# Optimization experiments

Hardware: AMD Instinct MI355X
Metric: run time of the kernel (lower is better)

Reference implementation:

```python
import jax, jax.numpy as jnp
import numpy as np

HIDDEN = 256
N_PROT = 12288
N_MOL = 6144
N_BATCH = 32


def setup_inputs() -> dict:
    key = jax.random.key(0)
    ks = jax.random.split(key, 10)
    s = 1.0 / np.sqrt(HIDDEN)  # torch Linear default init scale
    inp = {
        "prot_embed": jax.random.normal(ks[0], (N_PROT, HIDDEN), jnp.float32),
        "mol_embed": jax.random.normal(ks[1], (N_MOL, HIDDEN), jnp.float32),
        "prot_batch": jnp.sort(jax.random.randint(ks[2], (N_PROT,), 0, N_BATCH)),
        "mol_batch": jnp.sort(jax.random.randint(ks[3], (N_MOL,), 0, N_BATCH)),
        "Wq": jax.random.uniform(ks[4], (HIDDEN, HIDDEN), jnp.float32, -s, s),
        "bq": jax.random.uniform(ks[5], (HIDDEN,), jnp.float32, -s, s),
        "Wk": jax.random.uniform(ks[6], (HIDDEN, HIDDEN), jnp.float32, -s, s),
        "bk": jax.random.uniform(ks[7], (HIDDEN,), jnp.float32, -s, s),
        "Wv": jax.random.uniform(ks[8], (HIDDEN, HIDDEN), jnp.float32, -s, s),
        "bv": jax.random.uniform(ks[9], (HIDDEN,), jnp.float32, -s, s),
    }
    return inp


def reference(prot_embed, mol_embed, prot_batch, mol_batch, Wq, bq, Wk, bk, Wv, bv):
    # Linear projections (torch nn.Linear: x @ W.T + b)
    Q = prot_embed @ Wq.T + bq            # [N, H]
    K = mol_embed @ Wk.T + bk             # [M, H]
    V = mol_embed @ Wv.T + bv             # [M, H]

    scale = 1.0 / jnp.sqrt(jnp.asarray(Q.shape[-1], Q.dtype))
    scores = (Q @ K.T) * scale            # [N, M]

    # block mask: same-batch pairs only
    mask = prot_batch[:, None] == mol_batch[None, :]   # [N, M] bool
    neg_inf = jnp.asarray(-jnp.inf, scores.dtype)
    scores = jnp.where(mask, scores, neg_inf)

    # stable masked softmax; rows with no valid key -> all zeros
    # (matches torch softmax(-inf row) -> nan -> nan_to_num(0.0))
    row_any = mask.any(axis=-1, keepdims=True)
    mx = jnp.max(scores, axis=-1, keepdims=True)
    mx = jnp.where(row_any, mx, 0.0)
    e = jnp.exp(scores - mx)              # exp(-inf)=0 on masked entries
    denom = jnp.sum(e, axis=-1, keepdims=True)
    attn = e / jnp.where(row_any, denom, 1.0)  # [N, M]

    out = attn @ V                        # [N, H]
    return out, attn
```

## Files before the change

### kernel.cpp

```cpp
#include <hip/hip_runtime.h>

#define NPROT 12288
#define NMOL  6144
#define HID   256
#define NB    32

#define PROT_O 0
#define MOL_O  3145728
#define WQ_O   4718592
#define WK_O   4784128
#define WV_O   4849664
#define BQ_O   4915200
#define BK_O   4915456
#define BV_O   4915712
#define Q_O    4915968
#define K_O    8061696
#define VT_O   9634560
#define END_O  11207424

#define FROWS_BLK 49152

typedef __attribute__((ext_vector_type(4))) float f32x4;
typedef __attribute__((ext_vector_type(8))) short bf16x8;
typedef unsigned short u16;
typedef unsigned int   u32;

__device__ __forceinline__ float b2f(u16 u){
  union { u32 i; float f; } v; v.i = ((u32)u) << 16; return v.f;
}
__device__ __forceinline__ u16 f2b(float f){
  union { float fl; u32 i; } v; v.fl = f;
  u32 i = v.i;
  return (u16)((i + 0x7FFFu + ((i >> 16) & 1u)) >> 16);
}

__device__ __forceinline__ void fill_rows8(float* attnf, int fid){
  float* dst = attnf + (size_t)fid * FROWS_BLK + threadIdx.x * 4;
  f32x4 z = {0.f, 0.f, 0.f, 0.f};
  #pragma unroll 4
  for (int i = 0; i < 48; i++)
    __builtin_nontemporal_store(z, (f32x4*)(dst + i * 1024));
}

__global__ __launch_bounds__(256) void convert_kernel(
    const float* __restrict__ prot, const float* __restrict__ mol,
    const float* __restrict__ Wq, const float* __restrict__ Wk,
    const float* __restrict__ Wv, const float* __restrict__ bq,
    const float* __restrict__ bk, const float* __restrict__ bv,
    const int* __restrict__ pb, const int* __restrict__ mb,
    int* __restrict__ rg, u16* __restrict__ cvt, float* __restrict__ dout)
{
  if (blockIdx.x >= 4801){
    fill_rows8(dout + (size_t)NPROT * HID, blockIdx.x - 4801);
    return;
  }
  int g = blockIdx.x * 256 + threadIdx.x;
  const float* src = nullptr; u16* dst = nullptr; int off = 0;
  if      (g < 786432)  { src = prot; dst = cvt + PROT_O; off = g; }
  else if (g < 1179648) { src = mol;  dst = cvt + MOL_O;  off = g - 786432; }
  else if (g < 1196032) { src = Wq;   dst = cvt + WQ_O;   off = g - 1179648; }
  else if (g < 1212416) { src = Wk;   dst = cvt + WK_O;   off = g - 1196032; }
  else if (g < 1228800) { src = Wv;   dst = cvt + WV_O;   off = g - 1212416; }
  else if (g < 1228864) { src = bq;   dst = cvt + BQ_O;   off = g - 1228800; }
  else if (g < 1228928) { src = bk;   dst = cvt + BK_O;   off = g - 1228864; }
  else if (g < 1228992) { src = bv;   dst = cvt + BV_O;   off = g - 1228928; }
  if (src){
    f32x4 v = *(const f32x4*)(src + (size_t)off * 4);
    ushort4 o;
    o.x = f2b(v[0]); o.y = f2b(v[1]); o.z = f2b(v[2]); o.w = f2b(v[3]);
    *(ushort4*)(dst + (size_t)off * 4) = o;
  }

  if (blockIdx.x == 0 && threadIdx.x < 64){
    int t = threadIdx.x;
    const int* arr = (t < 32) ? pb : mb;
    int n          = (t < 32) ? NPROT : NMOL;
    int target     = (t & 31) + 1;
    int lo = 0, hi = n;
    while (lo < hi){
      int mid = (lo + hi) >> 1;
      if (arr[mid] < target) lo = mid + 1; else hi = mid;
    }
    int end = lo;
    int prev = __shfl(end, t - 1);
    int start = ((t & 31) == 0) ? 0 : prev;
    int b = t & 31;
    if (t < 32){ rg[b] = start; rg[32 + b] = end; }
    else       { rg[64 + b] = start; rg[96 + b] = end; }
  }
}

__global__ __launch_bounds__(256) void proj_kernel(
    const u16* __restrict__ cvt,
    u16* __restrict__ Q, u16* __restrict__ K, u16* __restrict__ Vt,
    float* __restrict__ dout)
{
  __shared__ u16 tlds[4][64][18];
  if (blockIdx.x >= 1536){
    fill_rows8(dout + (size_t)NPROT * HID, blockIdx.x - 1536 + 512);
    return;
  }
  int rowblk = blockIdx.x >> 2, colblk = blockIdx.x & 3;
  int proj;
  if      (rowblk < 192){ proj = 0; }
  else if (rowblk < 288){ proj = 1; rowblk -= 192; }
  else                  { proj = 2; rowblk -= 288; }
  const u16 *X, *W, *B;
  if (proj == 0){ X = cvt + PROT_O; W = cvt + WQ_O; B = cvt + BQ_O; }
  else if (proj == 1){ X = cvt + MOL_O; W = cvt + WK_O; B = cvt + BK_O; }
  else { X = cvt + MOL_O; W = cvt + WV_O; B = cvt + BV_O; }

  int wave = threadIdx.x >> 6, lane = threadIdx.x & 63;
  int m = lane & 15, q = lane >> 4;
  int rowbase = rowblk * 64 + wave * 16;
  int colbase = colblk * 64;

  const u16* arow = X + (size_t)(rowbase + m) * HID;
  f32x4 acc[4] = {};
  for (int k0 = 0; k0 < HID; k0 += 32){
    bf16x8 a = *(const bf16x8*)(arow + k0 + q*8);
    #pragma unroll
    for (int ct = 0; ct < 4; ct++){
      bf16x8 b = *(const bf16x8*)(W + (size_t)(colbase + ct*16 + m) * HID + k0 + q*8);
      acc[ct] = __builtin_amdgcn_mfma_f32_16x16x32_bf16(a, b, acc[ct], 0, 0, 0);
    }
  }

  if (proj < 2){
    u16* O = (proj == 0) ? Q : K;
    #pragma unroll
    for (int ct = 0; ct < 4; ct++){
      int col = colbase + ct*16 + m;
      float bb = b2f(B[col]);
      #pragma unroll
      for (int r = 0; r < 4; r++){
        int row = rowbase + q*4 + r;
        O[(size_t)row * HID + col] = f2b(acc[ct][r] + bb);
      }
    }
  } else {
    #pragma unroll
    for (int ct = 0; ct < 4; ct++){
      int lc = ct*16 + m;
      float bb = b2f(B[colbase + lc]);
      #pragma unroll
      for (int r = 0; r < 4; r++)
        tlds[wave][lc][q*4 + r] = f2b(acc[ct][r] + bb);
    }
    __syncthreads();
    int col = colbase + lane;
    u32 packed[8];
    #pragma unroll
    for (int i = 0; i < 8; i++){
      u16 lo = tlds[wave][lane][2*i];
      u16 hi = tlds[wave][lane][2*i+1];
      packed[i] = (u32)lo | ((u32)hi << 16);
    }
    u16* dst = Vt + (size_t)col * NMOL + rowbase;
    uint4 v0 = {packed[0], packed[1], packed[2], packed[3]};
    uint4 v1 = {packed[4], packed[5], packed[6], packed[7]};
    *(uint4*)dst = v0;
    *(uint4*)(dst + 8) = v1;
  }
}

__global__ __launch_bounds__(256) void attn_kernel(
    const int* __restrict__ rg, const int* __restrict__ pb,
    const u16* __restrict__ Q, const u16* __restrict__ K,
    const u16* __restrict__ Vt, float* __restrict__ dout)
{
  __shared__ u16 P[16][392];
  __shared__ float mxw[4][16];
  __shared__ float smw[4][16];
  const float scale = 0.0625f;
  float* outf  = dout;
  float* attnf = dout + (size_t)NPROT * HID;

  if (blockIdx.x >= 32){
    int fid = (blockIdx.x - 32) + 8 * blockIdx.y;
    int r0 = 8192 + fid * 16;
    f32x4 z = {0.f, 0.f, 0.f, 0.f};
    for (int rr = 0; rr < 16; rr++){
      int row = r0 + rr;
      int bb = pb[row];
      int ms = rg[64 + bb], me = rg[96 + bb];
      float* rowp = attnf + (size_t)row * NMOL;
      int mv = ms & ~3;
      for (int c = threadIdx.x * 4; c < mv; c += 1024)
        __builtin_nontemporal_store(z, (f32x4*)(rowp + c));
      for (int c = mv + threadIdx.x; c < ms; c += 256)
        rowp[c] = 0.f;
      int mu = (me + 3) & ~3;
      for (int c = me + threadIdx.x; c < mu && c < NMOL; c += 256)
        rowp[c] = 0.f;
      for (int c = mu + threadIdx.x * 4; c < NMOL; c += 1024)
        __builtin_nontemporal_store(z, (f32x4*)(rowp + c));
    }
    return;
  }

  int b = blockIdx.y;
  int ps = rg[b], pe = rg[32+b], ms = rg[64+b], me = rg[96+b];
  int Np = pe - ps, Nm = me - ms;
  if (Np <= 0) return;

  int wave = threadIdx.x >> 6, lane = threadIdx.x & 63;
  int m = lane & 15, q = lane >> 4;
  int ntiles = (Np + 15) >> 4;

  int bs = 0, ce = 0;
  if (Nm > 0){ bs = ms & ~31; ce = bs + ((me - bs + 31) & ~31); }

  for (int tile = blockIdx.x; tile < ntiles; tile += 32){
    int row0 = ps + tile * 16;
    int qr = min(row0 + m, NPROT - 1);
    const u16* qrow = Q + (size_t)qr * HID;
    bf16x8 qf[8];
    #pragma unroll
    for (int kk = 0; kk < 8; kk++)
      qf[kk] = *(const bf16x8*)(qrow + kk*32 + q*8);

    if (Nm > 0){
      int myj0 = bs + wave * 16;
      f32x4 sreg[6];
      float mx[4] = {-1e30f, -1e30f, -1e30f, -1e30f};
      #pragma unroll
      for (int c = 0; c < 6; c++){
        int j0 = myj0 + 64*c;
        if (j0 < ce){
          int col = j0 + m;
          bool valid = (col >= ms) && (col < me);
          const u16* krow = K + (size_t)col * HID;
          f32x4 s0 = {0.f,0.f,0.f,0.f}, s1 = {0.f,0.f,0.f,0.f};
          #pragma unroll
          for (int kk = 0; kk < 4; kk++){
            bf16x8 kb0 = *(const bf16x8*)(krow + kk*32 + q*8);
            bf16x8 kb1 = *(const bf16x8*)(krow + (kk+4)*32 + q*8);
            s0 = __builtin_amdgcn_mfma_f32_16x16x32_bf16(qf[kk],   kb0, s0, 0, 0, 0);
            s1 = __builtin_amdgcn_mfma_f32_16x16x32_bf16(qf[kk+4], kb1, s1, 0, 0, 0);
          }
          f32x4 sv;
          #pragma unroll
          for (int r = 0; r < 4; r++)
            sv[r] = valid ? (s0[r] + s1[r]) * scale : -1e30f;
          sreg[c] = sv;
          float cm[4];
          #pragma unroll
          for (int r = 0; r < 4; r++) cm[r] = sv[r];
          #pragma unroll
          for (int d = 1; d < 16; d <<= 1)
            #pragma unroll
            for (int r = 0; r < 4; r++)
              cm[r] = fmaxf(cm[r], __shfl_xor(cm[r], d, 16));
          #pragma unroll
          for (int r = 0; r < 4; r++) mx[r] = fmaxf(mx[r], cm[r]);
        }
      }
      if (m == 0){
        #pragma unroll
        for (int r = 0; r < 4; r++) mxw[wave][q*4 + r] = mx[r];
      }
      __syncthreads();
      float gmx[4];
      #pragma unroll
      for (int r = 0; r < 4; r++){
        int row = q*4 + r;
        float M = mxw[0][row];
        #pragma unroll
        for (int w = 1; w < 4; w++) M = fmaxf(M, mxw[w][row]);
        gmx[r] = M;
      }

      float sm[4] = {0.f, 0.f, 0.f, 0.f};
      #pragma unroll
      for (int c = 0; c < 6; c++){
        int j0 = myj0 + 64*c;
        if (j0 < ce){
          f32x4 e;
          #pragma unroll
          for (int r = 0; r < 4; r++) e[r] = __expf(sreg[c][r] - gmx[r]);
          sreg[c] = e;
          float t[4];
          #pragma unroll
          for (int r = 0; r < 4; r++) t[r] = e[r];
          #pragma unroll
          for (int d = 1; d < 16; d <<= 1)
            #pragma unroll
            for (int r = 0; r < 4; r++)
              t[r] += __shfl_xor(t[r], d, 16);
          #pragma unroll
          for (int r = 0; r < 4; r++) sm[r] += t[r];
        }
      }
      if (m == 0){
        #pragma unroll
        for (int r = 0; r < 4; r++) smw[wave][q*4 + r] = sm[r];
      }
      __syncthreads();
      float ginv[4];
      #pragma unroll
      for (int r = 0; r < 4; r++){
        int row = q*4 + r;
        float S = smw[0][row] + smw[1][row] + smw[2][row] + smw[3][row];
        ginv[r] = (S > 0.f) ? (1.f / S) : 0.f;
      }

      #pragma unroll
      for (int c = 0; c < 6; c++){
        int j0 = myj0 + 64*c;
        if (j0 < ce){
          int col = j0 + m;
          int jl = j0 - bs;
          bool valid = (col >= ms) && (col < me);
          #pragma unroll
          for (int r = 0; r < 4; r++){
            float p = sreg[c][r] * ginv[r];
            P[q*4 + r][jl + m] = f2b(p);
            int row = row0 + q*4 + r;
            if (valid && row < pe)
              __builtin_nontemporal_store(p, attnf + (size_t)row * NMOL + col);
          }
        }
      }
      __syncthreads();

      f32x4 oacc[4] = {};
      for (int j0 = bs; j0 < ce; j0 += 32){
        int jl = j0 - bs;
        bf16x8 a = *(const bf16x8*)(&P[m][jl + q*8]);
        #pragma unroll
        for (int c2 = 0; c2 < 4; c2++){
          int ct = wave*4 + c2;
          bf16x8 vb = *(const bf16x8*)(Vt + (size_t)(ct*16 + m) * NMOL + j0 + q*8);
          oacc[c2] = __builtin_amdgcn_mfma_f32_16x16x32_bf16(a, vb, oacc[c2], 0, 0, 0);
        }
      }
      #pragma unroll
      for (int c2 = 0; c2 < 4; c2++){
        int col = (wave*4 + c2)*16 + m;
        #pragma unroll
        for (int r = 0; r < 4; r++){
          int row = row0 + q*4 + r;
          if (row < pe) outf[(size_t)row * HID + col] = oacc[c2][r];
        }
      }
    } else {
      #pragma unroll
      for (int c2 = 0; c2 < 4; c2++){
        int col = (wave*4 + c2)*16 + m;
        #pragma unroll
        for (int r = 0; r < 4; r++){
          int row = row0 + q*4 + r;
          if (row < pe) outf[(size_t)row * HID + col] = 0.f;
        }
      }
    }
    __syncthreads();
  }
}

extern "C" void kernel_launch(void* const* d_in, const int* in_sizes, int n_in,
                              void* d_out, int out_size, void* d_ws, size_t ws_size,
                              hipStream_t stream)
{
  (void)in_sizes; (void)n_in; (void)out_size;
  const float* prot = (const float*)d_in[0];
  const float* mol  = (const float*)d_in[1];
  const int* pb     = (const int*)d_in[2];
  const int* mb     = (const int*)d_in[3];
  const float* Wq   = (const float*)d_in[4];
  const float* bq   = (const float*)d_in[5];
  const float* Wk   = (const float*)d_in[6];
  const float* bk   = (const float*)d_in[7];
  const float* Wv   = (const float*)d_in[8];
  const float* bv   = (const float*)d_in[9];

  const size_t need = 1024 + (size_t)END_O * 2;
  if (ws_size < need) return;

  char* ws = (char*)d_ws;
  int* rg  = (int*)ws;
  u16* cvt = (u16*)(ws + 1024);
  u16* Qp  = cvt + Q_O;
  u16* Kp  = cvt + K_O;
  u16* Vtp = cvt + VT_O;
  float* out = (float*)d_out;

  convert_kernel<<<dim3(4801 + 512), dim3(256), 0, stream>>>(
      prot, mol, Wq, Wk, Wv, bq, bk, bv, pb, mb, rg, cvt, out);
  proj_kernel<<<dim3(1536 + 512), dim3(256), 0, stream>>>(
      cvt, Qp, Kp, Vtp, out);
  attn_kernel<<<dim3(40, NB), dim3(256), 0, stream>>>(rg, pb, Qp, Kp, Vtp, out);
}
```

Measured before the change: 390.1 us.

## Fuse fp32-to-bf16 activation conversion into projection kernel via LDS staging

The separate conversion pass for prot and mol embeddings is removed. The projection kernel now loads fp32 rows directly, converts them to bf16 into shared memory, and each block computes all 256 output columns for 16 rows, with each wave covering 64 columns. This drops a full round trip of the converted activations through global memory and shrinks the prep kernel to weights, biases and fill work. In exchange, each block now reads the whole weight matrix, and the output tile shape and grid mapping change.

```diff
diff --git a/kernel.cpp b/kernel.cpp
--- a/kernel.cpp
+++ b/kernel.cpp
@@ -5,8 +5,6 @@
 #define HID   256
 #define NB    32
 
-#define PROT_O 0
-#define MOL_O  3145728
 #define WQ_O   4718592
 #define WK_O   4784128
 #define WV_O   4849664
@@ -42,28 +40,25 @@
     __builtin_nontemporal_store(z, (f32x4*)(dst + i * 1024));
 }
 
-__global__ __launch_bounds__(256) void convert_kernel(
-    const float* __restrict__ prot, const float* __restrict__ mol,
+__global__ __launch_bounds__(256) void prep_kernel(
     const float* __restrict__ Wq, const float* __restrict__ Wk,
     const float* __restrict__ Wv, const float* __restrict__ bq,
     const float* __restrict__ bk, const float* __restrict__ bv,
     const int* __restrict__ pb, const int* __restrict__ mb,
     int* __restrict__ rg, u16* __restrict__ cvt, float* __restrict__ dout)
 {
-  if (blockIdx.x >= 4801){
-    fill_rows8(dout + (size_t)NPROT * HID, blockIdx.x - 4801);
+  if (blockIdx.x < 512){
+    fill_rows8(dout + (size_t)NPROT * HID, blockIdx.x);
     return;
   }
-  int g = blockIdx.x * 256 + threadIdx.x;
+  int g = (blockIdx.x - 512) * 256 + threadIdx.x;
   const float* src = nullptr; u16* dst = nullptr; int off = 0;
-  if      (g < 786432)  { src = prot; dst = cvt + PROT_O; off = g; }
-  else if (g < 1179648) { src = mol;  dst = cvt + MOL_O;  off = g - 786432; }
-  else if (g < 1196032) { src = Wq;   dst = cvt + WQ_O;   off = g - 1179648; }
-  else if (g < 1212416) { src = Wk;   dst = cvt + WK_O;   off = g - 1196032; }
-  else if (g < 1228800) { src = Wv;   dst = cvt + WV_O;   off = g - 1212416; }
-  else if (g < 1228864) { src = bq;   dst = cvt + BQ_O;   off = g - 1228800; }
-  else if (g < 1228928) { src = bk;   dst = cvt + BK_O;   off = g - 1228864; }
-  else if (g < 1228992) { src = bv;   dst = cvt + BV_O;   off = g - 1228928; }
+  if      (g < 16384) { src = Wq; dst = cvt + WQ_O; off = g; }
+  else if (g < 32768) { src = Wk; dst = cvt + WK_O; off = g - 16384; }
+  else if (g < 49152) { src = Wv; dst = cvt + WV_O; off = g - 32768; }
+  else if (g < 49216) { src = bq; dst = cvt + BQ_O; off = g - 49152; }
+  else if (g < 49280) { src = bk; dst = cvt + BK_O; off = g - 49216; }
+  else if (g < 49344) { src = bv; dst = cvt + BV_O; off = g - 49280; }
   if (src){
     f32x4 v = *(const f32x4*)(src + (size_t)off * 4);
     ushort4 o;
@@ -71,7 +66,7 @@
     *(ushort4*)(dst + (size_t)off * 4) = o;
   }
 
-  if (blockIdx.x == 0 && threadIdx.x < 64){
+  if (blockIdx.x == 512 && threadIdx.x < 64){
     int t = threadIdx.x;
     const int* arr = (t < 32) ? pb : mb;
     int n          = (t < 32) ? NPROT : NMOL;
@@ -91,34 +86,53 @@
 }
 
 __global__ __launch_bounds__(256) void proj_kernel(
+    const float* __restrict__ prot, const float* __restrict__ mol,
     const u16* __restrict__ cvt,
     u16* __restrict__ Q, u16* __restrict__ K, u16* __restrict__ Vt,
     float* __restrict__ dout)
 {
+  __shared__ u16 xlds[16][264];
   __shared__ u16 tlds[4][64][18];
   if (blockIdx.x >= 1536){
     fill_rows8(dout + (size_t)NPROT * HID, blockIdx.x - 1536 + 512);
     return;
   }
-  int rowblk = blockIdx.x >> 2, colblk = blockIdx.x & 3;
+  int rb = blockIdx.x;
   int proj;
-  if      (rowblk < 192){ proj = 0; }
-  else if (rowblk < 288){ proj = 1; rowblk -= 192; }
-  else                  { proj = 2; rowblk -= 288; }
-  const u16 *X, *W, *B;
-  if (proj == 0){ X = cvt + PROT_O; W = cvt + WQ_O; B = cvt + BQ_O; }
-  else if (proj == 1){ X = cvt + MOL_O; W = cvt + WK_O; B = cvt + BK_O; }
-  else { X = cvt + MOL_O; W = cvt + WV_O; B = cvt + BV_O; }
+  const float* X; const u16 *W, *B;
+  if      (rb < 768) { proj = 0; X = prot; W = cvt + WQ_O; B = cvt + BQ_O; }
+  else if (rb < 1152){ proj = 1; rb -= 768;  X = mol; W = cvt + WK_O; B = cvt + BK_O; }
+  else               { proj = 2; rb -= 1152; X = mol; W = cvt + WV_O; B = cvt + BV_O; }
+  int rowbase = rb * 16;
+
+  {
+    int r  = threadIdx.x >> 4;
+    int c0 = (threadIdx.x & 15) * 16;
+    const float* xp = X + (size_t)(rowbase + r) * HID + c0;
+    f32x4 v0 = *(const f32x4*)(xp);
+    f32x4 v1 = *(const f32x4*)(xp + 4);
+    f32x4 v2 = *(const f32x4*)(xp + 8);
+    f32x4 v3 = *(const f32x4*)(xp + 12);
+    u16* d = &xlds[r][c0];
+    ushort4 o0, o1, o2, o3;
+    o0.x = f2b(v0[0]); o0.y = f2b(v0[1]); o0.z = f2b(v0[2]); o0.w = f2b(v0[3]);
+    o1.x = f2b(v1[0]); o1.y = f2b(v1[1]); o1.z = f2b(v1[2]); o1.w = f2b(v1[3]);
+    o2.x = f2b(v2[0]); o2.y = f2b(v2[1]); o2.z = f2b(v2[2]); o2.w = f2b(v2[3]);
+    o3.x = f2b(v3[0]); o3.y = f2b(v3[1]); o3.z = f2b(v3[2]); o3.w = f2b(v3[3]);
+    *(ushort4*)(d)      = o0;
+    *(ushort4*)(d + 4)  = o1;
+    *(ushort4*)(d + 8)  = o2;
+    *(ushort4*)(d + 12) = o3;
+  }
+  __syncthreads();
 
   int wave = threadIdx.x >> 6, lane = threadIdx.x & 63;
   int m = lane & 15, q = lane >> 4;
-  int rowbase = rowblk * 64 + wave * 16;
-  int colbase = colblk * 64;
-
-  const u16* arow = X + (size_t)(rowbase + m) * HID;
+  int colbase = wave * 64;
+
   f32x4 acc[4] = {};
   for (int k0 = 0; k0 < HID; k0 += 32){
-    bf16x8 a = *(const bf16x8*)(arow + k0 + q*8);
+    bf16x8 a = *(const bf16x8*)(&xlds[m][k0 + q*8]);
     #pragma unroll
     for (int ct = 0; ct < 4; ct++){
       bf16x8 b = *(const bf16x8*)(W + (size_t)(colbase + ct*16 + m) * HID + k0 + q*8);
@@ -386,9 +400,9 @@
   u16* Vtp = cvt + VT_O;
   float* out = (float*)d_out;
 
-  convert_kernel<<<dim3(4801 + 512), dim3(256), 0, stream>>>(
-      prot, mol, Wq, Wk, Wv, bq, bk, bv, pb, mb, rg, cvt, out);
+  prep_kernel<<<dim3(512 + 193), dim3(256), 0, stream>>>(
+      Wq, Wk, Wv, bq, bk, bv, pb, mb, rg, cvt, out);
   proj_kernel<<<dim3(1536 + 512), dim3(256), 0, stream>>>(
-      cvt, Qp, Kp, Vtp, out);
+      prot, mol, cvt, Qp, Kp, Vtp, out);
   attn_kernel<<<dim3(40, NB), dim3(256), 0, stream>>>(rg, pb, Qp, Kp, Vtp, out);
 }
```

Measured after the change: 390.9 us. Within noise of the previous version (+0.2%).
